# Kernel tuning notes

Measured on AMD Instinct MI355X. Metric: run time of the kernel, lower is better.

Reference implementation:

```python
import jax, jax.numpy as jnp
import numpy as np
from jax import lax

N_COMPONENTS = 50
K = 15
SIGMA = 1.0
N_ITERS = 100


def _pairwise_sq_dists(x):
    # squared euclidean distances, [N, N]
    sq = jnp.sum(x * x, axis=1)
    d2 = sq[:, None] + sq[None, :] - 2.0 * (x @ x.T)
    return jnp.maximum(d2, 0.0)


def _knn_affinity(d2, scale):
    # top-K smallest distances per row -> dense sparse-pattern affinity, row-normalized
    n = d2.shape[0]
    neg_topk, knn_idx = lax.top_k(-d2, K)          # [N, K]
    w = jnp.exp(-(-neg_topk) * scale)              # exp(-d^2 * scale) on kNN entries
    rows = jnp.arange(n)[:, None]
    mat = jnp.zeros_like(d2).at[rows, knn_idx].set(w)
    return mat / jnp.sum(mat, axis=1, keepdims=True)


def setup_inputs() -> dict:
    key = jax.random.key(0)
    expression = jax.random.normal(key, (4096, 1000), dtype=jnp.float32)
    return {"expression": expression}


def reference(expression):
    x = expression
    n = x.shape[0]

    # --- PCA via eigh of gene-gene covariance ---
    xc = x - jnp.mean(x, axis=0)
    cov = (xc.T @ xc) / (n - 1)                    # [G, G]
    evals, evecs = jnp.linalg.eigh(cov)            # ascending
    order = jnp.argsort(evals)[::-1]
    evecs = evecs[:, order]
    pca = xc @ evecs[:, :N_COMPONENTS]             # [N, C]

    d2 = _pairwise_sq_dists(pca)                   # [N, N]

    # transition matrix: exp(-d^2 / (2 sigma^2)) on kNN
    transition = _knn_affinity(d2, 1.0 / (2.0 * SIGMA ** 2))
    # pseudotime diffusion matrix: exp(-d^2) on kNN
    diff_mat = _knn_affinity(d2, 1.0)

    # power iteration from root cell 0
    d0 = jnp.zeros((n,), dtype=pca.dtype).at[0].set(1.0)

    def step(d, _):
        dn = diff_mat @ d
        dn = dn / jnp.max(dn)
        return dn, None

    pseudotime, _ = lax.scan(step, d0, None, length=N_ITERS)

    return (pseudotime.astype(jnp.float32),
            transition.astype(jnp.float32),
            pca.astype(jnp.float32))
```

## Files before the change

kernel.cpp:

```cpp
#include <hip/hip_runtime.h>
#include <math.h>
#include <stdint.h>

static const int NS = 4096;
static const int MF = 1000;
static const int NCOMP = 50;
#define AH_LD 1024

#define TR_OFF  ((size_t)4096)
#define PCA_OFF ((size_t)4096 + (size_t)4096*4096)
#define HH_GRID 250

__global__ void k_colsum(const float* __restrict__ x, float* __restrict__ part){
  int b = blockIdx.x, tid = threadIdx.x;
  float a0=0,a1=0,a2=0,a3=0;
  for (int r=b*64; r<b*64+64; r++){
    const float* row = x + (size_t)r*MF;
    if (tid      < MF) a0 += row[tid];
    if (tid+256  < MF) a1 += row[tid+256];
    if (tid+512  < MF) a2 += row[tid+512];
    if (tid+768  < MF) a3 += row[tid+768];
  }
  if (tid      < MF) part[b*MF+tid]     = a0;
  if (tid+256  < MF) part[b*MF+tid+256] = a1;
  if (tid+512  < MF) part[b*MF+tid+512] = a2;
  if (tid+768  < MF) part[b*MF+tid+768] = a3;
}

__global__ void k_colmean(const float* __restrict__ part, float* __restrict__ mean){
  int c = blockIdx.x*256 + threadIdx.x;
  if (c < MF){ float s=0; for (int b=0;b<64;b++) s += part[b*MF+c]; mean[c] = s/4096.0f; }
}

__global__ void k_barinit(unsigned long long* bar){ if (threadIdx.x==0) *bar = 0ull; }

__global__ void k_cov(const float* __restrict__ x, const float* __restrict__ mean,
                      double* __restrict__ Ah){
  __shared__ float As[32][65];
  __shared__ float Bs[32][65];
  int bx = blockIdx.x, by = blockIdx.y;
  if (bx > by) return;
  int i0 = by*64, j0 = bx*64;
  int tx = threadIdx.x, ty = threadIdx.y;
  int tid = ty*16+tx;
  double acc[4][4];
  #pragma unroll
  for (int u=0;u<4;u++)
    #pragma unroll
    for (int v=0;v<4;v++) acc[u][v]=0.0;
  for (int k0=0;k0<4096;k0+=32){
    for (int t=tid;t<32*64;t+=256){
      int kk=t>>6, ii=t&63;
      int gi=i0+ii, gj=j0+ii;
      As[kk][ii] = (gi<MF) ? (x[(size_t)(k0+kk)*MF+gi]-mean[gi]) : 0.f;
      Bs[kk][ii] = (gj<MF) ? (x[(size_t)(k0+kk)*MF+gj]-mean[gj]) : 0.f;
    }
    __syncthreads();
    for (int kk=0;kk<32;kk++){
      float a[4], b[4];
      #pragma unroll
      for (int u=0;u<4;u++){ a[u]=As[kk][ty*4+u]; b[u]=Bs[kk][tx*4+u]; }
      #pragma unroll
      for (int u=0;u<4;u++)
        #pragma unroll
        for (int v=0;v<4;v++) acc[u][v] += (double)a[u]*(double)b[v];
    }
    __syncthreads();
  }
  #pragma unroll
  for (int u=0;u<4;u++)
    #pragma unroll
    for (int v=0;v<4;v++){
      int gi=i0+ty*4+u, gj=j0+tx*4+v;
      if (gi<MF && gj<MF){
        double val = acc[u][v]*(1.0/4095.0);
        Ah[(size_t)gi*AH_LD+gj] = val;
        Ah[(size_t)gj*AH_LD+gi] = val;
      }
    }
}

__device__ __forceinline__ unsigned wang(unsigned s){
  s=(s^61u)^(s>>16); s*=9u; s^=s>>4; s*=0x27d4eb2du; s^=s>>15; return s;
}

__device__ __forceinline__ double cohLoadD(const double* p){
  unsigned long long v = __hip_atomic_load((const unsigned long long*)p,
      __ATOMIC_RELAXED, __HIP_MEMORY_SCOPE_AGENT);
  return __longlong_as_double((long long)v);
}
__device__ __forceinline__ void cohStoreD(double* p, double v){
  __hip_atomic_store((unsigned long long*)p,
      (unsigned long long)__double_as_longlong(v),
      __ATOMIC_RELAXED, __HIP_MEMORY_SCOPE_AGENT);
}

__device__ __forceinline__ void grid_sync_fast(unsigned long long* bar){
  __syncthreads();
  if (threadIdx.x == 0){
    asm volatile("s_waitcnt vmcnt(0)" ::: "memory");
    unsigned long long old = __hip_atomic_fetch_add(bar, 1ull,
        __ATOMIC_RELAXED, __HIP_MEMORY_SCOPE_AGENT);
    if ((unsigned)(old & 0xffffffffull) == (unsigned)(HH_GRID-1)){
      __hip_atomic_fetch_add(bar, (1ull<<32) - (unsigned long long)HH_GRID,
          __ATOMIC_RELAXED, __HIP_MEMORY_SCOPE_AGENT);
    } else {
      unsigned gen = (unsigned)(old >> 32);
      while ((unsigned)(__hip_atomic_load(bar, __ATOMIC_RELAXED,
                 __HIP_MEMORY_SCOPE_AGENT) >> 32) == gen)
        __builtin_amdgcn_s_sleep(1);
    }
  }
  __syncthreads();
}

__global__ void __launch_bounds__(256) k_hh_all(double* Ah,
                                                double* __restrict__ Vh,
                                                double* __restrict__ tauv,
                                                double* __restrict__ betaH,
                                                double* w1a, double* w1b,
                                                double* cola, double* colb,
                                                unsigned long long* bar){
  __shared__ double vbuf[2][1000];
  __shared__ double wfull[1000];
  __shared__ double red4[4], redb[4];
  __shared__ double sAlpha;
  int tid = threadIdx.x;
  int lane = tid & 63, wv = tid >> 6;
  int bid = blockIdx.x;
  int myrow = bid + wv*HH_GRID;
  double tau_prev = 0.0;

  for (int k = 0; k < 998; k++){
    double* vk    = vbuf[k & 1];
    double* vprev = vbuf[(k & 1) ^ 1];
    const double* w1prev  = (k & 1) ? w1a : w1b;
    double*       w1next  = (k & 1) ? w1b : w1a;
    const double* colprev = (k & 1) ? cola : colb;
    double*       colnext = (k & 1) ? colb : cola;

    double vd = 0.0;
    if (k > 0){
      for (int j = k + tid; j < 1000; j += 256){
        double ww = cohLoadD(&w1prev[j]);
        wfull[j] = ww;
        vd += vprev[j]*ww;
      }
    }
    #pragma unroll
    for (int off=32; off; off>>=1) vd += __shfl_down(vd, off, 64);
    if (lane==0) red4[wv] = vd;
    __syncthreads();
    double vdot = red4[0]+red4[1]+red4[2]+red4[3];
    double tp  = tau_prev;
    double hts = 0.5*tp*tp*vdot;
    if (k > 0){
      for (int j = k + tid; j < 1000; j += 256)
        wfull[j] = tp*wfull[j] - hts*vprev[j];
    }
    __syncthreads();

    double a2 = 0.0;
    for (int j = k+1 + tid; j < 1000; j += 256){
      double c;
      if (k > 0) c = cohLoadD(&colprev[j]) - (vprev[j]*wfull[k] + wfull[j]*vprev[k]);
      else       c = Ah[(size_t)j*AH_LD + k];
      vk[j] = c;
      if (j == k+1) sAlpha = c;
      if (j > k+1) a2 += c*c;
    }
    #pragma unroll
    for (int off=32; off; off>>=1) a2 += __shfl_down(a2, off, 64);
    if (lane==0) redb[wv] = a2;
    __syncthreads();
    double xn2 = redb[0]+redb[1]+redb[2]+redb[3];
    double alpha = sAlpha;
    double beta, tau, scl;
    if (xn2 == 0.0){ beta = alpha; tau = 0.0; scl = 0.0; }
    else {
      double nrm = sqrt(alpha*alpha + xn2);
      beta = (alpha >= 0.0) ? -nrm : nrm;
      tau  = (beta - alpha)/beta;
      scl  = 1.0/(alpha - beta);
    }
    if (tid==0){
      if (bid==0){ tauv[k]=tau; betaH[k]=beta; }
      if (k>0 && bid == (k % HH_GRID)) Ah[(size_t)k*AH_LD + k] -= 2.0*wfull[k];
    }
    for (int j = k+1 + tid; j < 1000; j += 256)
      vk[j] = (j == k+1) ? 1.0 : vk[j]*scl;
    __syncthreads();
    if (bid==0){
      for (int j = k+1 + tid; j < 1000; j += 256)
        Vh[(size_t)k*MF + j] = vk[j];
    }

    int r = myrow;
    if (r >= k+1 && r < 1000){
      double vr = (k>0)? vprev[r] : 0.0;
      double wr = (k>0)? wfull[r] : 0.0;
      double* row = Ah + (size_t)r*AH_LD;
      double acc = 0.0;
      for (int c = k+1 + lane; c < 1000; c += 64){
        double a = row[c];
        if (k > 0){ a -= vr*wfull[c] + wr*vprev[c]; row[c] = a; }
        acc += a*vk[c];
        if (c == k+1) cohStoreD(&colnext[r], a);
      }
      #pragma unroll
      for (int off=32; off; off>>=1) acc += __shfl_down(acc, off, 64);
      if (lane==0) cohStoreD(&w1next[r], acc);
    }

    grid_sync_fast(bar);
    tau_prev = tau;
  }
}

__device__ __forceinline__ int sgnchg(double a, double b){
  return (int)(((unsigned long long)(__double_as_longlong(a) ^ __double_as_longlong(b))) >> 63);
}

__global__ void k_post(double* __restrict__ Ah, const double* __restrict__ Vh,
                       const double* __restrict__ tauv, const double* __restrict__ w1last,
                       double* __restrict__ alphaH, double* __restrict__ betaH,
                       double* __restrict__ lamT){
  __shared__ double al[1000], abv[1000], bb[1000];
  int tid = threadIdx.x;
  if (tid==0){
    double v8 = Vh[(size_t)997*MF + 998];
    double v9 = Vh[(size_t)997*MF + 999];
    double w18 = w1last[998], w19 = w1last[999];
    double tau = tauv[997];
    double vdot = v8*w18 + v9*w19;
    double hts = 0.5*tau*tau*vdot;
    double w8 = tau*w18 - hts*v8;
    double w9 = tau*w19 - hts*v9;
    Ah[(size_t)998*AH_LD+998] -= v8*w8 + w8*v8;
    Ah[(size_t)999*AH_LD+998] -= v9*w8 + w9*v8;
    Ah[(size_t)999*AH_LD+999] -= v9*w9 + w9*v9;
  }
  __syncthreads();
  for (int t=tid;t<1000;t+=64){
    double a2 = Ah[(size_t)t*AH_LD+t];
    alphaH[t]=a2; al[t]=a2;
  }
  if (tid==0) betaH[998] = Ah[(size_t)999*AH_LD+998];
  __syncthreads();
  for (int t=tid;t<1000;t+=64){
    double b = (t<999)? betaH[t] : 0.0;
    abv[t]=fabs(b); bb[t]=b*b;
  }
  __syncthreads();
  if (tid >= NCOMP) return;
  int i = tid;
  double lo=1e300, hi=-1e300;
  for (int k2=0;k2<1000;k2++){
    double bl = (k2>0)? abv[k2-1] : 0.0;
    double br = (k2<999)? abv[k2] : 0.0;
    double a = al[k2];
    lo = fmin(lo, a-bl-br);
    hi = fmax(hi, a+bl+br);
  }
  int target = 999 - i;
  for (int it=0; it<55; it++){
    double mid = 0.5*(lo+hi);
    int cnt = 0;
    double d1 = 1.0;
    double d0 = al[0]-mid;
    cnt += (int)(((unsigned long long)__double_as_longlong(d0))>>63);
    int k2 = 1;
    for (; k2+3 < 1000; k2 += 4){
      double n0 = (al[k2  ]-mid)*d0 - bb[k2-1]*d1;
      double n1 = (al[k2+1]-mid)*n0 - bb[k2  ]*d0;
      double n2 = (al[k2+2]-mid)*n1 - bb[k2+1]*n0;
      double n3 = (al[k2+3]-mid)*n2 - bb[k2+2]*n1;
      cnt += sgnchg(n0,d0)+sgnchg(n1,n0)+sgnchg(n2,n1)+sgnchg(n3,n2);
      double mm = fmax(fabs(n3), fabs(n2));
      double s = (mm > 1e250) ? 1e-250 : ((mm < 1e-250) ? 1e250 : 1.0);
      d1 = n2*s; d0 = n3*s;
    }
    for (; k2 < 1000; k2++){
      double nn = (al[k2]-mid)*d0 - bb[k2-1]*d1;
      cnt += sgnchg(nn, d0);
      d1 = d0; d0 = nn;
    }
    if (cnt > target) hi = mid; else lo = mid;
  }
  lamT[i] = 0.5*(lo+hi);
}

__device__ void gtsv_serial(int m, double* dl, double* dd, double* du, double* x){
  for (int r=0;r<m-1;r++){
    if (fabs(dd[r]) >= fabs(dl[r])){
      if (dd[r] != 0.0){
        double fact = dl[r]/dd[r];
        dd[r+1] -= fact*du[r];
        x[r+1]  -= fact*x[r];
      }
      if (r < m-2) dl[r] = 0.0;
    } else {
      double fact = dd[r]/dl[r];
      dd[r] = dl[r];
      double tdd = dd[r+1];
      dd[r+1] = du[r] - fact*tdd;
      if (r < m-2){
        double tdu = du[r+1];
        dl[r] = tdu;
        du[r+1] = -fact*tdu;
      }
      du[r] = tdd;
      double t2 = x[r]; x[r] = x[r+1]; x[r+1] = t2 - fact*x[r+1];
    }
  }
  x[m-1] /= dd[m-1];
  if (m >= 2) x[m-2] = (x[m-2] - du[m-2]*x[m-1])/dd[m-2];
  for (int r=m-3;r>=0;r--)
    x[r] = (x[r] - du[r]*x[r+1] - dl[r]*x[r+2])/dd[r];
}

__global__ void __launch_bounds__(256) k_invsign(const double* __restrict__ alphaH,
                                                 const double* __restrict__ betaH,
                                                 const double* __restrict__ lamT,
                                                 double* __restrict__ V50,
                                                 float* __restrict__ sgnv){
  __shared__ double v[1000], xx[1000], dd[1000], du[1000], dl[1000];
  __shared__ double red[256];
  __shared__ double lam_s;
  __shared__ int ab[2];
  __shared__ float sig;
  int i = blockIdx.x, tid = threadIdx.x;
  double lam = lamT[i];
  for (int t=tid;t<1000;t+=256){
    unsigned h = wang((unsigned)(i*1000+t)*2654435761u + 777u);
    v[t] = (double)(h & 0xffffffu)/8388608.0 - 1.0;
  }
  __syncthreads();
  for (int it=0; it<3; it++){
    for (int t=tid;t<1000;t+=256){
      dd[t] = alphaH[t]-lam;
      if (t<999){ du[t]=betaH[t]; dl[t]=betaH[t]; }
      xx[t] = v[t];
    }
    __syncthreads();
    if (tid==0) gtsv_serial(1000, dl, dd, du, xx);
    __syncthreads();
    double a=0; for (int t=tid;t<1000;t+=256) a += xx[t]*xx[t];
    red[tid]=a; __syncthreads();
    for (int off=128;off;off>>=1){ if(tid<off) red[tid]+=red[tid+off]; __syncthreads(); }
    double inv = 1.0/sqrt(red[0]);
    __syncthreads();
    for (int t=tid;t<1000;t+=256) v[t]=xx[t]*inv;
    __syncthreads();
  }
  double a=0;
  for (int t=tid;t<1000;t+=256){
    double s = alphaH[t]*v[t];
    if (t>0)   s += betaH[t-1]*v[t-1];
    if (t<999) s += betaH[t]*v[t+1];
    a += v[t]*s;
  }
  red[tid]=a; __syncthreads();
  for (int off=128;off;off>>=1){ if(tid<off) red[tid]+=red[tid+off]; __syncthreads(); }
  if (tid==0){ lam_s = red[0]; ab[0]=0; ab[1]=1000; sig=1.f; }
  for (int t=tid;t<1000;t+=256) V50[(size_t)i*1000+t]=v[t];
  __syncthreads();
  while (true){
    int a0=ab[0], b0=ab[1];
    if (b0-a0 <= 25) break;
    int c = a0 + (b0-a0)/2;
    double m1=0,m2=0;
    for (int t=a0+tid;t<b0;t+=256){ double q=v[t]*v[t]; if (t<c) m1+=q; else m2+=q; }
    red[tid]=m1; __syncthreads();
    for (int off=128;off;off>>=1){ if(tid<off) red[tid]+=red[tid+off]; __syncthreads(); }
    double M1=red[0]; __syncthreads();
    red[tid]=m2; __syncthreads();
    for (int off=128;off;off>>=1){ if(tid<off) red[tid]+=red[tid+off]; __syncthreads(); }
    double M2=red[0]; __syncthreads();
    double tot=M1+M2;
    if (fmin(M1,M2) <= 1e-10*tot){
      if (tid==0){ if (M1>=M2) ab[1]=c; else ab[0]=c; }
      __syncthreads();
      a0=ab[0]; b0=ab[1];
      double nn=0; for (int t=a0+tid;t<b0;t+=256) nn+=v[t]*v[t];
      red[tid]=nn; __syncthreads();
      for (int off=128;off;off>>=1){ if(tid<off) red[tid]+=red[tid+off]; __syncthreads(); }
      double inv = 1.0/sqrt(red[0]); __syncthreads();
      for (int t=a0+tid;t<b0;t+=256) v[t]*=inv;
      __syncthreads();
      for (int it=0; it<2; it++){
        for (int t=a0+tid;t<b0;t+=256){
          int L=t-a0;
          dd[L]=alphaH[t]-lam_s;
          if (t<b0-1){ du[L]=betaH[t]; dl[L]=betaH[t]; }
          xx[L]=v[t];
        }
        __syncthreads();
        if (tid==0) gtsv_serial(b0-a0, dl, dd, du, xx);
        __syncthreads();
        double s2=0; for (int t=a0+tid;t<b0;t+=256){ double q=xx[t-a0]; s2+=q*q; }
        red[tid]=s2; __syncthreads();
        for (int off=128;off;off>>=1){ if(tid<off) red[tid]+=red[tid+off]; __syncthreads(); }
        double inv2 = 1.0/sqrt(red[0]); __syncthreads();
        for (int t=a0+tid;t<b0;t+=256) v[t]=xx[t-a0]*inv2;
        __syncthreads();
      }
      double rq=0;
      for (int t=a0+tid;t<b0;t+=256){
        double s = alphaH[t]*v[t];
        if (t>a0)   s += betaH[t-1]*v[t-1];
        if (t<b0-1) s += betaH[t]*v[t+1];
        rq += v[t]*s;
      }
      red[tid]=rq; __syncthreads();
      for (int off=128;off;off>>=1){ if(tid<off) red[tid]+=red[tid+off]; __syncthreads(); }
      if (tid==0) lam_s=red[0];
      __syncthreads();
      continue;
    }
    if (tid==0){
      double vc1 = v[c-1], vc = v[c];
      if (fabs(vc1) >= fabs(vc)){
        sig = (vc1 < 0.0) ? 1.f : -1.f;
      } else {
        double req = (betaH[c-1] >= 0.0) ? -1.0 : 1.0;
        double have = (vc >= 0.0) ? 1.0 : -1.0;
        sig = (have == req) ? 1.f : -1.f;
      }
    }
    break;
  }
  __syncthreads();
  if (tid==0) sgnv[i]=sig;
}

__global__ void __launch_bounds__(256) k_applyQm(const double* __restrict__ Vh,
                                                 const double* __restrict__ tauv,
                                                 const double* __restrict__ V50,
                                                 const float* __restrict__ sgnv,
                                                 float* __restrict__ E50){
  __shared__ double red2[2][4];
  __shared__ double tl[1000];
  int i = blockIdx.x, tid = threadIdx.x;
  int lane = tid & 63, wv = tid >> 6;
  int base = tid*4;
  for (int t=tid;t<1000;t+=256) tl[t] = tauv[t];
  const double* src = V50 + (size_t)i*1000;
  double u0=0,u1=0,u2=0,u3=0;
  if (base < 1000){
    u0 = src[base]; u1 = src[base+1]; u2 = src[base+2]; u3 = src[base+3];
  }
  __syncthreads();
  for (int k=997;k>=0;k--){
    const double* v = Vh + (size_t)k*MF;
    double a = 0.0, v0=0,v1=0,v2=0,v3=0;
    if (base < 1000 && base+3 >= k+1){
      if (base   >= k+1){ v0 = v[base  ]; a += v0*u0; }
      if (base+1 >= k+1){ v1 = v[base+1]; a += v1*u1; }
      if (base+2 >= k+1){ v2 = v[base+2]; a += v2*u2; }
      if (base+3 >= k+1){ v3 = v[base+3]; a += v3*u3; }
    }
    #pragma unroll
    for (int off=32; off; off>>=1) a += __shfl_down(a, off, 64);
    if (lane==0) red2[k&1][wv] = a;
    __syncthreads();
    double td = tl[k]*(red2[k&1][0]+red2[k&1][1]+red2[k&1][2]+red2[k&1][3]);
    u0 -= td*v0; u1 -= td*v1; u2 -= td*v2; u3 -= td*v3;
  }
  double s = (double)sgnv[i];
  if (base < 1000){
    E50[(size_t)(base  )*NCOMP + i] = (float)(u0*s);
    E50[(size_t)(base+1)*NCOMP + i] = (float)(u1*s);
    E50[(size_t)(base+2)*NCOMP + i] = (float)(u2*s);
    E50[(size_t)(base+3)*NCOMP + i] = (float)(u3*s);
  }
}

__global__ void k_pca(const float* __restrict__ x, const float* __restrict__ mean,
                      const float* __restrict__ E, float* __restrict__ P){
  __shared__ float As[64][65];
  __shared__ float Es[64][65];
  int r0 = blockIdx.x*64;
  int tx = threadIdx.x & 15, ty = threadIdx.x >> 4;
  float acc[4][4];
  #pragma unroll
  for (int u=0;u<4;u++)
    #pragma unroll
    for (int v=0;v<4;v++) acc[u][v]=0.f;
  for (int k0=0;k0<MF;k0+=64){
    for (int t=threadIdx.x;t<64*64;t+=256){
      int i=t>>6, kk=t&63; int k=k0+kk;
      As[i][kk] = (k<MF) ? (x[(size_t)(r0+i)*MF+k]-mean[k]) : 0.f;
    }
    for (int t=threadIdx.x;t<64*65;t+=256){
      int kk=t/65, c=t%65; int k=k0+kk;
      Es[kk][c] = (k<MF && c<NCOMP) ? E[(size_t)k*NCOMP+c] : 0.f;
    }
    __syncthreads();
    for (int kk=0;kk<64;kk++){
      float a[4], b[4];
      #pragma unroll
      for (int u=0;u<4;u++){ a[u]=As[ty*4+u][kk]; b[u]=Es[kk][tx*4+u]; }
      #pragma unroll
      for (int u=0;u<4;u++)
        #pragma unroll
        for (int v=0;v<4;v++) acc[u][v] += a[u]*b[v];
    }
    __syncthreads();
  }
  #pragma unroll
  for (int u=0;u<4;u++){
    int r=r0+ty*4+u;
    #pragma unroll
    for (int v=0;v<4;v++){
      int c=tx*4+v;
      if (c<NCOMP) P[(size_t)r*NCOMP+c] = acc[u][v];
    }
  }
}

__global__ void k_rowsq(const float* __restrict__ P, float* __restrict__ sqv){
  int r = blockIdx.x*256 + threadIdx.x;
  if (r < NS){
    float s=0;
    for (int c=0;c<NCOMP;c++){ float v=P[(size_t)r*NCOMP+c]; s+=v*v; }
    sqv[r]=s;
  }
}

__global__ void k_knn(const float* __restrict__ P, const float* __restrict__ sqv,
                      float* __restrict__ trans, int* __restrict__ kidx,
                      float* __restrict__ kwd){
  __shared__ float pi[64];
  __shared__ unsigned long long keys[16*256];
  __shared__ unsigned long long redk[4];
  __shared__ unsigned long long wink[15];
  __shared__ float wt[15], wd[15], sums[2];
  int i = blockIdx.x, tid = threadIdx.x;
  int lane = tid & 63, wv = tid >> 6;
  for (int t=tid;t<NCOMP;t+=256) pi[t] = P[(size_t)i*NCOMP+t];
  __syncthreads();
  float sqi = sqv[i];
  for (int s2=0;s2<16;s2++){
    int j = tid + s2*256;
    float dot=0;
    for (int c=0;c<NCOMP;c++) dot += pi[c]*P[(size_t)j*NCOMP+c];
    float d2 = sqi + sqv[j] - 2.f*dot;
    d2 = fmaxf(d2, 0.f);
    unsigned int db = __float_as_uint(d2);
    keys[s2*256+tid] = ((unsigned long long)db<<32) | (unsigned)j;
  }
  __syncthreads();
  for (int rsel=0;rsel<15;rsel++){
    unsigned long long m = ~0ull;
    #pragma unroll
    for (int s2=0;s2<16;s2++){
      unsigned long long k = keys[s2*256+tid];
      m = (k<m)?k:m;
    }
    #pragma unroll
    for (int off=32; off; off>>=1){
      unsigned long long o = __shfl_down(m, off, 64);
      m = (o<m)?o:m;
    }
    if (lane==0) redk[wv]=m;
    __syncthreads();
    unsigned long long w = redk[0];
    if (redk[1]<w) w=redk[1];
    if (redk[2]<w) w=redk[2];
    if (redk[3]<w) w=redk[3];
    if (tid==0) wink[rsel]=w;
    #pragma unroll
    for (int s2=0;s2<16;s2++)
      if (keys[s2*256+tid]==w) keys[s2*256+tid]=~0ull;
    __syncthreads();
  }
  if (tid<15){
    unsigned long long w = wink[tid];
    float d2 = __uint_as_float((unsigned)(w>>32));
    wt[tid] = expf(-0.5f*d2);
    wd[tid] = expf(-d2);
  }
  __syncthreads();
  if (tid==0){
    float st=0, sd=0;
    for (int k=0;k<15;k++){ st+=wt[k]; sd+=wd[k]; }
    sums[0]=st; sums[1]=sd;
  }
  __syncthreads();
  float* row = trans + (size_t)i*NS;
  for (int c=tid;c<NS;c+=256) row[c]=0.f;
  __syncthreads();
  if (tid<15){
    int j = (int)(wink[tid] & 0xffffffffull);
    row[j] = wt[tid]/sums[0];
    kidx[i*15+tid] = j;
    kwd[i*15+tid]  = wd[tid]/sums[1];
  }
}

__global__ void __launch_bounds__(1024) k_power(const int* __restrict__ kidx,
                                                const float* __restrict__ kwd,
                                                float* __restrict__ outPT){
  __shared__ float d[4096];
  __shared__ float dn[4096];
  __shared__ float red[16];
  int tid = threadIdx.x;
  int lane = tid & 63, wv = tid >> 6;
  for (int t=tid;t<4096;t+=1024) d[t] = (t==0)?1.f:0.f;
  __syncthreads();
  for (int it=0; it<100; it++){
    float lmax = 0.f;
    for (int r=tid;r<4096;r+=1024){
      float a=0;
      #pragma unroll
      for (int k=0;k<15;k++) a += kwd[r*15+k]*d[kidx[r*15+k]];
      dn[r]=a;
      lmax = fmaxf(lmax, a);
    }
    #pragma unroll
    for (int off=32; off; off>>=1) lmax = fmaxf(lmax, __shfl_down(lmax, off, 64));
    if (lane==0) red[wv]=lmax;
    __syncthreads();
    float m = red[0];
    #pragma unroll
    for (int w=1;w<16;w++) m = fmaxf(m, red[w]);
    for (int r=tid;r<4096;r+=1024) d[r]=dn[r]/m;
    __syncthreads();
  }
  for (int t=tid;t<4096;t+=1024) outPT[t]=d[t];
}

extern "C" void kernel_launch(void* const* d_in, const int* in_sizes, int n_in,
                              void* d_out, int out_size, void* d_ws, size_t ws_size,
                              hipStream_t stream){
  const float* x = (const float*)d_in[0];
  float* out = (float*)d_out;
  char* base = (char*)d_ws;

  double* Ah     = (double*)(base + 0);
  float*  sqv    = (float*) (base + 0);
  int*    kidx   = (int*)   (base + 16384);
  float*  kwd    = (float*) (base + 262144);
  double* Vh     = (double*)(base + 8192000);
  double* V50    = (double*)(base + 16192000);
  float*  E50    = (float*) (base + 16592000);
  float*  part   = (float*) (base + 16792000);
  float*  mean   = (float*) (base + 17048000);
  double* tauv   = (double*)(base + 17052000);
  double* betaH  = (double*)(base + 17060000);
  double* alphaH = (double*)(base + 17068000);
  double* w1a    = (double*)(base + 17076000);
  double* w1b    = (double*)(base + 17084000);
  double* cola   = (double*)(base + 17092000);
  double* colb   = (double*)(base + 17100000);
  double* lamT   = (double*)(base + 17108000);
  float*  sgnv   = (float*) (base + 17108400);
  unsigned long long* bar = (unsigned long long*)(base + 17108600);

  k_colsum<<<64,256,0,stream>>>(x, part);
  k_colmean<<<4,256,0,stream>>>(part, mean);
  k_barinit<<<1,64,0,stream>>>(bar);
  k_cov<<<dim3(16,16),dim3(16,16),0,stream>>>(x, mean, Ah);

  k_hh_all<<<HH_GRID,256,0,stream>>>(Ah, Vh, tauv, betaH, w1a, w1b, cola, colb, bar);

  k_post<<<1,64,0,stream>>>(Ah, Vh, tauv, w1b, alphaH, betaH, lamT);

  k_invsign<<<50,256,0,stream>>>(alphaH, betaH, lamT, V50, sgnv);

  k_applyQm<<<50,256,0,stream>>>(Vh, tauv, V50, sgnv, E50);
  k_pca<<<64,256,0,stream>>>(x, mean, E50, out + PCA_OFF);
  k_rowsq<<<16,256,0,stream>>>(out + PCA_OFF, sqv);
  k_knn<<<4096,256,0,stream>>>(out + PCA_OFF, sqv, out + TR_OFF, kidx, kwd);
  k_power<<<1,1024,0,stream>>>(kidx, kwd, out);
}
```

Measured before the change: 17.34 ms.

## Replace atomic-counter grid barrier with per-block flags and master gather; vectorize power loop

Replaces the single-counter atomic grid barrier in the Householder tridiagonalization kernel with a flag-based barrier. Each block writes its own padded flag, block 0 polls all flags with one wavefront and then publishes a generation counter. This removes contended atomic fetch-adds on one address across the 997 barriers. Separately, the kNN index and weight arrays are padded to 16 entries per row so the power iteration can load them as float4/int4 vectors. The barrier relies on relaxed atomics plus waitcnt for memory ordering, which carries some visibility risk.

```diff
diff --git a/kernel.cpp b/kernel.cpp
--- a/kernel.cpp
+++ b/kernel.cpp
@@ -32,7 +32,11 @@
   if (c < MF){ float s=0; for (int b=0;b<64;b++) s += part[b*MF+c]; mean[c] = s/4096.0f; }
 }
 
-__global__ void k_barinit(unsigned long long* bar){ if (threadIdx.x==0) *bar = 0ull; }
+__global__ void k_barinit(unsigned* flags, unsigned* gen){
+  int t = threadIdx.x;
+  if (t < HH_GRID) flags[t*16] = 0u;
+  if (t == 255) *gen = 0u;
+}
 
 __global__ void k_cov(const float* __restrict__ x, const float* __restrict__ mean,
                       double* __restrict__ Ah){
@@ -94,24 +98,11 @@
       (unsigned long long)__double_as_longlong(v),
       __ATOMIC_RELAXED, __HIP_MEMORY_SCOPE_AGENT);
 }
-
-__device__ __forceinline__ void grid_sync_fast(unsigned long long* bar){
-  __syncthreads();
-  if (threadIdx.x == 0){
-    asm volatile("s_waitcnt vmcnt(0)" ::: "memory");
-    unsigned long long old = __hip_atomic_fetch_add(bar, 1ull,
-        __ATOMIC_RELAXED, __HIP_MEMORY_SCOPE_AGENT);
-    if ((unsigned)(old & 0xffffffffull) == (unsigned)(HH_GRID-1)){
-      __hip_atomic_fetch_add(bar, (1ull<<32) - (unsigned long long)HH_GRID,
-          __ATOMIC_RELAXED, __HIP_MEMORY_SCOPE_AGENT);
-    } else {
-      unsigned gen = (unsigned)(old >> 32);
-      while ((unsigned)(__hip_atomic_load(bar, __ATOMIC_RELAXED,
-                 __HIP_MEMORY_SCOPE_AGENT) >> 32) == gen)
-        __builtin_amdgcn_s_sleep(1);
-    }
-  }
-  __syncthreads();
+__device__ __forceinline__ unsigned cohLoadU(const unsigned* p){
+  return __hip_atomic_load(p, __ATOMIC_RELAXED, __HIP_MEMORY_SCOPE_AGENT);
+}
+__device__ __forceinline__ void cohStoreU(unsigned* p, unsigned v){
+  __hip_atomic_store(p, v, __ATOMIC_RELAXED, __HIP_MEMORY_SCOPE_AGENT);
 }
 
 __global__ void __launch_bounds__(256) k_hh_all(double* Ah,
@@ -120,7 +111,7 @@
                                                 double* __restrict__ betaH,
                                                 double* w1a, double* w1b,
                                                 double* cola, double* colb,
-                                                unsigned long long* bar){
+                                                unsigned* flags, unsigned* gen){
   __shared__ double vbuf[2][1000];
   __shared__ double wfull[1000];
   __shared__ double red4[4], redb[4];
@@ -212,7 +203,38 @@
       if (lane==0) cohStoreD(&w1next[r], acc);
     }
 
-    grid_sync_fast(bar);
+    if (k < 997){
+      unsigned target = (unsigned)(k+1);
+      asm volatile("s_waitcnt vmcnt(0)" ::: "memory");
+      __syncthreads();
+      if (bid == 0){
+        if (wv == 0){
+          for(;;){
+            unsigned mn = 0xffffffffu;
+            for (int b = 1 + lane; b < HH_GRID; b += 64){
+              unsigned f = cohLoadU(&flags[b*16]);
+              if (f < mn) mn = f;
+            }
+            #pragma unroll
+            for (int off=32; off; off>>=1){
+              unsigned o = (unsigned)__shfl_down((int)mn, off, 64);
+              if (o < mn) mn = o;
+            }
+            mn = (unsigned)__shfl((int)mn, 0, 64);
+            if (mn >= target) break;
+            __builtin_amdgcn_s_sleep(1);
+          }
+          if (lane==0) cohStoreU(gen, target);
+        }
+        __syncthreads();
+      } else {
+        if (tid==0){
+          cohStoreU(&flags[bid*16], target);
+          while (cohLoadU(gen) < target) __builtin_amdgcn_s_sleep(1);
+        }
+        __syncthreads();
+      }
+    }
     tau_prev = tau;
   }
 }
@@ -591,11 +613,16 @@
   float* row = trans + (size_t)i*NS;
   for (int c=tid;c<NS;c+=256) row[c]=0.f;
   __syncthreads();
-  if (tid<15){
-    int j = (int)(wink[tid] & 0xffffffffull);
-    row[j] = wt[tid]/sums[0];
-    kidx[i*15+tid] = j;
-    kwd[i*15+tid]  = wd[tid]/sums[1];
+  if (tid<16){
+    if (tid<15){
+      int j = (int)(wink[tid] & 0xffffffffull);
+      row[j] = wt[tid]/sums[0];
+      kidx[i*16+tid] = j;
+      kwd[i*16+tid]  = wd[tid]/sums[1];
+    } else {
+      kidx[i*16+15] = 0;
+      kwd[i*16+15]  = 0.f;
+    }
   }
 }
 
@@ -611,10 +638,18 @@
   __syncthreads();
   for (int it=0; it<100; it++){
     float lmax = 0.f;
-    for (int r=tid;r<4096;r+=1024){
-      float a=0;
-      #pragma unroll
-      for (int k=0;k<15;k++) a += kwd[r*15+k]*d[kidx[r*15+k]];
+    #pragma unroll
+    for (int s=0;s<4;s++){
+      int r = tid + s*1024;
+      const float4* wp = (const float4*)(kwd + (size_t)r*16);
+      const int4*   ip = (const int4*)  (kidx + (size_t)r*16);
+      float4 w0=wp[0], w1=wp[1], w2=wp[2], w3=wp[3];
+      int4   i0=ip[0], i1=ip[1], i2=ip[2], i3=ip[3];
+      float a = 0.f;
+      a += w0.x*d[i0.x]; a += w0.y*d[i0.y]; a += w0.z*d[i0.z]; a += w0.w*d[i0.w];
+      a += w1.x*d[i1.x]; a += w1.y*d[i1.y]; a += w1.z*d[i1.z]; a += w1.w*d[i1.w];
+      a += w2.x*d[i2.x]; a += w2.y*d[i2.y]; a += w2.z*d[i2.z]; a += w2.w*d[i2.w];
+      a += w3.x*d[i3.x]; a += w3.y*d[i3.y]; a += w3.z*d[i3.z]; a += w3.w*d[i3.w];
       dn[r]=a;
       lmax = fmaxf(lmax, a);
     }
@@ -641,7 +676,7 @@
   double* Ah     = (double*)(base + 0);
   float*  sqv    = (float*) (base + 0);
   int*    kidx   = (int*)   (base + 16384);
-  float*  kwd    = (float*) (base + 262144);
+  float*  kwd    = (float*) (base + 278528);
   double* Vh     = (double*)(base + 8192000);
   double* V50    = (double*)(base + 16192000);
   float*  E50    = (float*) (base + 16592000);
@@ -656,14 +691,16 @@
   double* colb   = (double*)(base + 17100000);
   double* lamT   = (double*)(base + 17108000);
   float*  sgnv   = (float*) (base + 17108400);
-  unsigned long long* bar = (unsigned long long*)(base + 17108600);
+  unsigned* gen  = (unsigned*)(base + 17200000);
+  unsigned* flags= (unsigned*)(base + 17200064);
 
   k_colsum<<<64,256,0,stream>>>(x, part);
   k_colmean<<<4,256,0,stream>>>(part, mean);
-  k_barinit<<<1,64,0,stream>>>(bar);
+  k_barinit<<<1,256,0,stream>>>(flags, gen);
   k_cov<<<dim3(16,16),dim3(16,16),0,stream>>>(x, mean, Ah);
 
-  k_hh_all<<<HH_GRID,256,0,stream>>>(Ah, Vh, tauv, betaH, w1a, w1b, cola, colb, bar);
+  k_hh_all<<<HH_GRID,256,0,stream>>>(Ah, Vh, tauv, betaH, w1a, w1b, cola, colb,
+                                     flags, gen);
 
   k_post<<<1,64,0,stream>>>(Ah, Vh, tauv, w1b, alphaH, betaH, lamT);
 
```

New measurement: 14.84 ms. 1.17x faster.
